# Optimization experiments

Hardware: AMD Instinct MI355X
Metric: run time of the kernel (lower is better)

Reference implementation:

```python
import jax, jax.numpy as jnp
import numpy as np
import math

DIM = 4096
N_HEADS = 32
HEAD_DIM = DIM // N_HEADS  # 128
SEQLEN = 2048


def setup_inputs() -> dict:
    key = jax.random.key(0)
    ks = jax.random.split(key, 8)
    x = jax.random.normal(ks[0], (1, SEQLEN, DIM), dtype=jnp.float32)
    # freqs_cis as real view: (seqlen, head_dim//2, 2) = (cos, sin) of rotary angles
    theta = 10000.0 ** (-jnp.arange(0, HEAD_DIM, 2, dtype=jnp.float32) / HEAD_DIM)
    angles = jnp.arange(SEQLEN, dtype=jnp.float32)[:, None] * theta[None, :]
    freqs = jnp.stack([jnp.cos(angles), jnp.sin(angles)], axis=-1)  # (S, 64, 2)
    # causal additive mask (use -1e9 instead of -inf for numeric safety)
    mask = jnp.triu(jnp.full((SEQLEN, SEQLEN), -1e9, dtype=jnp.float32), k=1)[None, None]
    scale = 1.0 / math.sqrt(DIM)
    wq = jax.random.normal(ks[1], (DIM, DIM), dtype=jnp.float32) * scale
    wk = jax.random.normal(ks[2], (DIM, DIM), dtype=jnp.float32) * scale
    wv = jax.random.normal(ks[3], (DIM, DIM), dtype=jnp.float32) * scale
    wo = jax.random.normal(ks[4], (DIM, DIM), dtype=jnp.float32) * scale
    return {"x": x, "start_pos": 0, "freqs": freqs, "mask": mask,
            "wq": wq, "wk": wk, "wv": wv, "wo": wo}


def _rotary(xq, xk, freqs, seqlen, n_heads, head_dim):
    # Faithful to source: note the repo's slice(0, 2) means xq_ == xq (no pair swap).
    ll = freqs[:, :, 0:1]  # (S, hd/2, 1) cos
    rr = freqs[:, :, 1:2]  # (S, hd/2, 1) sin
    fl = jnp.concatenate([ll, ll], axis=-1).reshape(seqlen, 1, head_dim)
    fr = jnp.concatenate([-rr, rr], axis=-1).reshape(seqlen, 1, head_dim)
    xq_ = xq.reshape(seqlen, n_heads, head_dim // 2, 2).reshape(seqlen, n_heads, head_dim)  # == xq
    xk_ = xk.reshape(seqlen, n_heads, head_dim // 2, 2).reshape(seqlen, n_heads, head_dim)  # == xk
    return xq * fl + xq_ * fr, xk * fl + xk_ * fr


def reference(x, start_pos, freqs, mask, wq, wk, wv, wo):
    bsz, seqlen, dim = x.shape  # bsz == 1 (source squeezes batch)
    xs = x[0]  # (S, D) -- HE encrypt/linear/decrypt roundtrip == plain linear
    xq = xs @ wq.T
    xk = xs @ wk.T
    xv = xs @ wv.T
    xq = xq.reshape(seqlen, N_HEADS, HEAD_DIM)
    xk = xk.reshape(seqlen, N_HEADS, HEAD_DIM)
    xv = xv.reshape(seqlen, N_HEADS, HEAD_DIM)
    xq, xk = _rotary(xq, xk, freqs, seqlen, N_HEADS, HEAD_DIM)
    # start_pos == 0 and zero-initialized cache => keys/values are just xk/xv
    q = jnp.transpose(xq, (1, 0, 2))  # (H, S, Dh)
    k = jnp.transpose(xk, (1, 0, 2))
    v = jnp.transpose(xv, (1, 0, 2))
    scores = jnp.einsum('hqd,hkd->hqk', q, k) / math.sqrt(HEAD_DIM)  # (H, S, S)
    scores = scores[None] + mask  # (1, H, S, S)
    probs = jax.nn.softmax(scores, axis=-1)
    out = jnp.einsum('bhqk,hkd->bhqd', probs, v)  # (1, H, S, Dh)
    out = jnp.transpose(out, (0, 2, 1, 3)).reshape(bsz, seqlen, dim)
    return out @ wo.T
```

## Files before the change

kernel.cpp:

```cpp
#include <hip/hip_runtime.h>

#define DIM 4096
#define SEQ 2048
#define NH 32
#define HD 128

typedef __bf16 bf16x8 __attribute__((ext_vector_type(8)));
typedef float f32x4 __attribute__((ext_vector_type(4)));

#define QSCALE 0.12751649736765598f

__device__ inline ushort f2bf(float f) {
    union { float f; unsigned u; } v; v.f = f;
    unsigned r = v.u + 0x7fffu + ((v.u >> 16) & 1u);
    return (ushort)(r >> 16);
}

__global__ void conv_all(const float* __restrict__ x,  const float* __restrict__ wq,
                         const float* __restrict__ wk, const float* __restrict__ wv,
                         const float* __restrict__ wo,
                         ushort* __restrict__ xb,  ushort* __restrict__ wqb,
                         ushort* __restrict__ wkb, ushort* __restrict__ wvb,
                         ushort* __restrict__ wob) {
    int i = blockIdx.x * 256 + threadIdx.x;
    const float* src; ushort* dst; int off;
    const int n4x = (SEQ * DIM) / 4;
    if (i < n4x) { src = x; dst = xb; off = i; }
    else {
        int j = i - n4x;
        int w = j >> 22;
        off = j & ((1 << 22) - 1);
        src = (w == 0) ? wq : (w == 1) ? wk : (w == 2) ? wv : wo;
        dst = (w == 0) ? wqb : (w == 1) ? wkb : (w == 2) ? wvb : wob;
    }
    float4 v = ((const float4*)src)[off];
    ushort4 o;
    o.x = f2bf(v.x); o.y = f2bf(v.y); o.z = f2bf(v.z); o.w = f2bf(v.w);
    ((ushort4*)dst)[off] = o;
}


#define AS1(p) (const __attribute__((address_space(1))) void*)(p)
#define AS3(p) (__attribute__((address_space(3))) void*)(p)
#define FENCE() asm volatile("" ::: "memory")
#define BARRIER() do { FENCE(); __builtin_amdgcn_s_barrier(); FENCE(); } while (0)

__device__ __forceinline__ void gemm256_body(
    const ushort* __restrict__ Ab,
    const ushort* __restrict__ Bb,
    ushort* __restrict__ sA0, ushort* __restrict__ sA1,
    ushort* __restrict__ sB0, ushort* __restrict__ sB1,
    f32x4 acc[8][4], const int K)
{
    const int tid  = threadIdx.x;
    const int wave = tid >> 6, lane = tid & 63;
    const int quad = lane >> 4, c = lane & 15;
    const int wm = wave >> 2, wn = wave & 3;

    const int aoff  = (lane >> 3) * K + (((lane & 7) ^ (lane >> 3)) * 8);
    const int sa_r0 = wave * 8;
    const int sb_r0 = (wave >> 1) * 64 + (wave & 1) * 16;

    const int rp0 = (quad ^ (c & 7)) * 8;
    const int rp1 = ((4 + quad) ^ (c & 7)) * 8;
    const int arow = (wm * 128 + c) * 64;
    const int brow = (wn * 64 + c) * 64;

#define STAGE_A(dst, h, k0) do { \
    const int _r0 = (h) * 64 + sa_r0; \
    __builtin_amdgcn_global_load_lds(AS1(Ab + (size_t)_r0 * K + (k0) + aoff), \
                                     AS3((dst) + _r0 * 64), 16, 0, 0); \
    const int _r1 = _r0 + 128; \
    __builtin_amdgcn_global_load_lds(AS1(Ab + (size_t)_r1 * K + (k0) + aoff), \
                                     AS3((dst) + _r1 * 64), 16, 0, 0); \
  } while (0)
#define STAGE_B(dst, h, k0) do { \
    const int _r0 = (h) * 32 + sb_r0; \
    __builtin_amdgcn_global_load_lds(AS1(Bb + (size_t)_r0 * K + (k0) + aoff), \
                                     AS3((dst) + _r0 * 64), 16, 0, 0); \
    const int _r1 = _r0 + 8; \
    __builtin_amdgcn_global_load_lds(AS1(Bb + (size_t)_r1 * K + (k0) + aoff), \
                                     AS3((dst) + _r1 * 64), 16, 0, 0); \
  } while (0)

    bf16x8 af[4][2], bfr[4][2];

#define READ_A(buf, mh) do { \
    _Pragma("unroll") \
    for (int _m = 0; _m < 4; ++_m) { \
        af[_m][0] = *(const bf16x8*)&(buf)[arow + (mh) * 4096 + _m * 1024 + rp0]; \
        af[_m][1] = *(const bf16x8*)&(buf)[arow + (mh) * 4096 + _m * 1024 + rp1]; \
    } } while (0)
#define READ_B2(buf, nh) do { \
    _Pragma("unroll") \
    for (int _n = 0; _n < 2; ++_n) { \
        bfr[(nh) * 2 + _n][0] = *(const bf16x8*)&(buf)[brow + (nh) * 2048 + _n * 1024 + rp0]; \
        bfr[(nh) * 2 + _n][1] = *(const bf16x8*)&(buf)[brow + (nh) * 2048 + _n * 1024 + rp1]; \
    } } while (0)
#define MMA_Q(mh, nq) do { \
    __builtin_amdgcn_s_setprio(1); \
    _Pragma("unroll") \
    for (int _kk = 0; _kk < 2; ++_kk) \
    _Pragma("unroll") \
    for (int _m = 0; _m < 4; ++_m) \
    _Pragma("unroll") \
    for (int _n = 0; _n < 2; ++_n) \
        acc[(mh) * 4 + _m][(nq) * 2 + _n] = __builtin_amdgcn_mfma_f32_16x16x32_bf16( \
            af[_m][_kk], bfr[(nq) * 2 + _n][_kk], acc[(mh) * 4 + _m][(nq) * 2 + _n], 0, 0, 0); \
    __builtin_amdgcn_s_setprio(0); \
  } while (0)

    const int NT = K >> 6;

    STAGE_A(sA0, 0, 0);  STAGE_A(sA0, 1, 0);
    STAGE_B(sB0, 0, 0);  STAGE_B(sB0, 1, 0);
    STAGE_A(sA1, 0, 64); STAGE_A(sA1, 1, 64);
    STAGE_B(sB1, 0, 64); STAGE_B(sB1, 1, 64);
    asm volatile("s_waitcnt vmcnt(8)" ::: "memory");
    BARRIER();

#pragma unroll 1
    for (int t = 0; t < NT; ++t) {
        ushort* cA = (t & 1) ? sA1 : sA0;
        ushort* cB = (t & 1) ? sB1 : sB0;
        const int kn2 = (t + 2) << 6;
        const bool ok2 = (t + 2 < NT);

        READ_A(cA, 0); READ_B2(cB, 0);
        BARRIER();
        MMA_Q(0, 0);
        BARRIER();

        READ_B2(cB, 1);
        if (ok2) { STAGE_A(cA, 0, kn2); STAGE_B(cB, 0, kn2); }
        BARRIER();
        MMA_Q(0, 1);
        BARRIER();

        READ_A(cA, 1);
        if (ok2) STAGE_B(cB, 1, kn2);
        BARRIER();
        MMA_Q(1, 0);
        BARRIER();

        if (ok2) STAGE_A(cA, 1, kn2);
        BARRIER();
        MMA_Q(1, 1);
        if (t < NT - 1) {
            if (ok2) asm volatile("s_waitcnt vmcnt(8)" ::: "memory");
            else     asm volatile("s_waitcnt vmcnt(0)" ::: "memory");
        }
        BARRIER();
    }
#undef STAGE_A
#undef STAGE_B
#undef READ_A
#undef READ_B2
#undef MMA_Q
}

__global__ __launch_bounds__(512, 2)
void gemm_qkv(const ushort* __restrict__ A,
              const ushort* __restrict__ Bq, const ushort* __restrict__ Bk,
              const ushort* __restrict__ Bv,
              ushort* __restrict__ qout, ushort* __restrict__ kout,
              ushort* __restrict__ vt, const float* __restrict__ freqs) {
    __shared__ __align__(16) ushort sA[2][256 * 64];
    __shared__ __align__(16) ushort sB[2][256 * 64];
    const int bi = blockIdx.x;
    const int x = bi & 7;
    const int l = bi >> 3;
    const int mblk = l & 7;
    const int nblk = x * 6 + (l >> 3);
    const int wsel = nblk >> 4;
    const int nloc = (nblk & 15) * 256;
    const int m0 = mblk * 256;
    const ushort* B = (wsel == 0) ? Bq : (wsel == 1) ? Bk : Bv;

    const f32x4 vzero = {0.f, 0.f, 0.f, 0.f};
    f32x4 acc[8][4];
#pragma unroll
    for (int i = 0; i < 8; i++)
#pragma unroll
        for (int j = 0; j < 4; j++) acc[i][j] = vzero;

    gemm256_body(A + (size_t)m0 * DIM, B + (size_t)nloc * DIM,
                 &sA[0][0], &sA[1][0], &sB[0][0], &sB[1][0], acc, DIM);

    const int tid = threadIdx.x;
    const int wave = tid >> 6, lane = tid & 63;
    const int quad = lane >> 4, c = lane & 15;
    const int wm = wave >> 2, wn = wave & 3;

    if (wsel < 2) {
        ushort* Cw = wsel ? kout : qout;
        const float qs = wsel ? 1.0f : QSCALE;
#pragma unroll
        for (int i = 0; i < 8; i++) {
#pragma unroll
            for (int j = 0; j < 4; j++) {
                int colg = nloc + wn * 64 + j * 16 + c;
                int dh = (colg & 127) >> 1;
#pragma unroll
                for (int r = 0; r < 4; r++) {
                    int row = m0 + wm * 128 + i * 16 + quad * 4 + r;
                    float2 f2 = ((const float2*)freqs)[row * 64 + dh];
                    float f = (f2.x + ((c & 1) ? f2.y : -f2.y)) * qs;
                    Cw[(size_t)row * DIM + colg] = f2bf(acc[i][j][r] * f);
                }
            }
        }
    } else {
#pragma unroll
        for (int i = 0; i < 8; i++) {
#pragma unroll
            for (int j = 0; j < 4; j++) {
                int cv = nloc + wn * 64 + j * 16 + c;
                int row0 = m0 + wm * 128 + i * 16 + quad * 4;
                ushort4 o;
                o.x = f2bf(acc[i][j][0]); o.y = f2bf(acc[i][j][1]);
                o.z = f2bf(acc[i][j][2]); o.w = f2bf(acc[i][j][3]);
                *(ushort4*)&vt[(size_t)cv * SEQ + row0] = o;
            }
        }
    }
}

__global__ __launch_bounds__(512, 2)
void gemm_f32out(const ushort* __restrict__ A, const ushort* __restrict__ B,
                 float* __restrict__ C, int M, int N, int K) {
    __shared__ __align__(16) ushort sA[2][256 * 64];
    __shared__ __align__(16) ushort sB[2][256 * 64];
    const int bi = blockIdx.x;
    const int x = bi & 7;
    const int l = bi >> 3;
    const int mblk = l & 7;
    const int nblk = x * 2 + (l >> 3);
    const int m0 = mblk * 256, n0 = nblk * 256;

    const f32x4 vzero = {0.f, 0.f, 0.f, 0.f};
    f32x4 acc[8][4];
#pragma unroll
    for (int i = 0; i < 8; i++)
#pragma unroll
        for (int j = 0; j < 4; j++) acc[i][j] = vzero;

    gemm256_body(A + (size_t)m0 * K, B + (size_t)n0 * K,
                 &sA[0][0], &sA[1][0], &sB[0][0], &sB[1][0], acc, K);

    const int tid = threadIdx.x;
    const int wave = tid >> 6, lane = tid & 63;
    const int quad = lane >> 4, c = lane & 15;
    const int wm = wave >> 2, wn = wave & 3;

#pragma unroll
    for (int i = 0; i < 8; i++)
#pragma unroll
        for (int j = 0; j < 4; j++)
#pragma unroll
            for (int r = 0; r < 4; r++) {
                int row = m0 + wm * 128 + i * 16 + quad * 4 + r;
                int col = n0 + wn * 64 + j * 16 + c;
                C[(size_t)row * N + col] = acc[i][j][r];
            }
}

__global__ __launch_bounds__(256)
void flash_kernel(const ushort* __restrict__ Q, const ushort* __restrict__ K,
                  const ushort* __restrict__ Vt, ushort* __restrict__ O) {
    const int bi = blockIdx.x;
    const int h = bi & (NH - 1);
    const int p = bi >> 5;
    __shared__ __align__(16) ushort sK[64 * 128];
    __shared__ __align__(16) ushort sVt[128 * 64];
    __shared__ __align__(16) ushort sP[4][16 * 72];
    const int tid = threadIdx.x, wave = tid >> 6, lane = tid & 63;
    const int quad = lane >> 4, c = lane & 15;

    for (int pass = 0; pass < 2; pass++) {
        const int qb = pass ? (SEQ / 64 - 1 - p) : p;
        const int q0 = qb * 64;

        bf16x8 qf[4];
        {
            const ushort* Qp = Q + (size_t)(q0 + wave * 16 + c) * DIM + h * HD;
#pragma unroll
            for (int ks = 0; ks < 4; ks++) qf[ks] = *(const bf16x8*)(Qp + ks * 32 + quad * 8);
        }
        const f32x4 vzero = {0.f, 0.f, 0.f, 0.f};
        f32x4 oa[8];
#pragma unroll
        for (int dt = 0; dt < 8; dt++) oa[dt] = vzero;
        float ms[4], ls[4];
#pragma unroll
        for (int r = 0; r < 4; r++) { ms[r] = -1e30f; ls[r] = 0.f; }

        for (int kt = 0; kt <= qb; kt++) {
            __syncthreads();
#pragma unroll
            for (int i = 0; i < 4; i++) {
                int lr = wave * 16 + i * 4 + (lane >> 4);
                int ch = lane & 15;
                int g = (ch & 8) | ((ch ^ lr) & 7);
                __builtin_amdgcn_global_load_lds(
                    (const __attribute__((address_space(1))) void*)(K + (size_t)(kt * 64 + lr) * DIM + h * HD + g * 8),
                    (__attribute__((address_space(3))) void*)(&sK[(wave * 16 + i * 4) * 128]), 16, 0, 0);
            }
#pragma unroll
            for (int i = 0; i < 4; i++) {
                int ld = wave * 32 + i * 8 + (lane >> 3);
                int ch = lane & 7;
                int g = (ch ^ ld) & 7;
                __builtin_amdgcn_global_load_lds(
                    (const __attribute__((address_space(1))) void*)(Vt + (size_t)(h * HD + ld) * SEQ + kt * 64 + g * 8),
                    (__attribute__((address_space(3))) void*)(&sVt[(wave * 32 + i * 8) * 64]), 16, 0, 0);
            }
            __syncthreads();

            f32x4 s[4];
#pragma unroll
            for (int nt = 0; nt < 4; nt++) s[nt] = vzero;
#pragma unroll
            for (int ks = 0; ks < 4; ks++)
#pragma unroll
                for (int nt = 0; nt < 4; nt++) {
                    int lr = nt * 16 + c;
                    int gc = ks * 4 + quad;
                    int pch = (gc & 8) | ((gc ^ lr) & 7);
                    bf16x8 kf = *(const bf16x8*)&sK[lr * 128 + pch * 8];
                    s[nt] = __builtin_amdgcn_mfma_f32_16x16x32_bf16(qf[ks], kf, s[nt], 0, 0, 0);
                }

            if (kt == qb) {
#pragma unroll
                for (int nt = 0; nt < 4; nt++)
#pragma unroll
                    for (int r = 0; r < 4; r++) {
                        int keyg = nt * 16 + c;
                        int qg   = wave * 16 + quad * 4 + r;
                        if (keyg > qg) s[nt][r] = -1e30f;
                    }
            }

            float mnew[4], alpha[4];
#pragma unroll
            for (int r = 0; r < 4; r++) {
                float v = fmaxf(fmaxf(s[0][r], s[1][r]), fmaxf(s[2][r], s[3][r]));
                v = fmaxf(v, __shfl_xor(v, 1));
                v = fmaxf(v, __shfl_xor(v, 2));
                v = fmaxf(v, __shfl_xor(v, 4));
                v = fmaxf(v, __shfl_xor(v, 8));
                mnew[r]  = fmaxf(ms[r], v);
                alpha[r] = exp2f(ms[r] - mnew[r]);
                ms[r]    = mnew[r];
            }
            float rs[4] = {0.f, 0.f, 0.f, 0.f};
#pragma unroll
            for (int nt = 0; nt < 4; nt++)
#pragma unroll
                for (int r = 0; r < 4; r++) {
                    float pv = exp2f(s[nt][r] - mnew[r]);
                    rs[r] += pv;
                    sP[wave][(quad * 4 + r) * 72 + nt * 16 + c] = f2bf(pv);
                }
#pragma unroll
            for (int r = 0; r < 4; r++) {
                float v = rs[r];
                v += __shfl_xor(v, 1);
                v += __shfl_xor(v, 2);
                v += __shfl_xor(v, 4);
                v += __shfl_xor(v, 8);
                ls[r] = ls[r] * alpha[r] + v;
            }
#pragma unroll
            for (int dt = 0; dt < 8; dt++)
#pragma unroll
                for (int r = 0; r < 4; r++) oa[dt][r] *= alpha[r];

            __asm__ volatile("s_waitcnt lgkmcnt(0)" ::: "memory");

#pragma unroll
            for (int k2 = 0; k2 < 2; k2++) {
                bf16x8 pf = *(const bf16x8*)&sP[wave][c * 72 + k2 * 32 + quad * 8];
#pragma unroll
                for (int dt = 0; dt < 8; dt++) {
                    int ld = dt * 16 + c;
                    int gc = k2 * 4 + quad;
                    int pch = (gc ^ ld) & 7;
                    bf16x8 vf = *(const bf16x8*)&sVt[ld * 64 + pch * 8];
                    oa[dt] = __builtin_amdgcn_mfma_f32_16x16x32_bf16(pf, vf, oa[dt], 0, 0, 0);
                }
            }
        }

#pragma unroll
        for (int r = 0; r < 4; r++) {
            float inv = 1.f / ls[r];
            int row = q0 + wave * 16 + quad * 4 + r;
#pragma unroll
            for (int dt = 0; dt < 8; dt++)
                O[(size_t)row * DIM + h * HD + dt * 16 + c] = f2bf(oa[dt][r] * inv);
        }
    }
}

extern "C" void kernel_launch(void* const* d_in, const int* in_sizes, int n_in,
                              void* d_out, int out_size, void* d_ws, size_t ws_size,
                              hipStream_t stream) {
    const float* x     = (const float*)d_in[0];
    const float* freqs = (const float*)d_in[2];
    const float* wq    = (const float*)d_in[4];
    const float* wk    = (const float*)d_in[5];
    const float* wv    = (const float*)d_in[6];
    const float* wo    = (const float*)d_in[7];
    float* out = (float*)d_out;

    ushort* xb    = (ushort*)d_ws;
    ushort* wqb   = xb    + (size_t)SEQ * DIM;
    ushort* wkb   = wqb   + (size_t)DIM * DIM;
    ushort* wvb   = wkb   + (size_t)DIM * DIM;
    ushort* wob   = wvb   + (size_t)DIM * DIM;
    ushort* qbuf  = wob   + (size_t)DIM * DIM;
    ushort* kbuf  = qbuf  + (size_t)SEQ * DIM;
    ushort* vtbuf = kbuf  + (size_t)SEQ * DIM;
    ushort* obuf  = vtbuf + (size_t)SEQ * DIM;

    const int n4tot = (SEQ * DIM + 4 * DIM * DIM) / 4;
    conv_all<<<n4tot / 256, 256, 0, stream>>>(x, wq, wk, wv, wo, xb, wqb, wkb, wvb, wob);

    gemm_qkv<<<dim3(384), 512, 0, stream>>>(xb, wqb, wkb, wvb, qbuf, kbuf, vtbuf, freqs);

    flash_kernel<<<dim3(NH * SEQ / 128), 256, 0, stream>>>(qbuf, kbuf, vtbuf, obuf);

    gemm_f32out<<<dim3(128), 512, 0, stream>>>(obuf, wob, out, SEQ, DIM, DIM);
}
```

Before: 759.3 us.

## Double-buffer K/V tiles in flash attention and raise MFMA wave priority

Gives the flash attention kernel two LDS buffers for K and V^T. The next key tile is prefetched with global_load_lds while the current tile is being computed, and partial vmcnt waits replace the per-iteration load-then-sync pattern. This is meant to hide global-memory latency behind the QK^T and PV MFMA work. It also wraps the MFMA loops in s_setprio so waves issue matrix work ahead of others. The cost is double the K/V LDS footprint, which may reduce the number of blocks resident per CU.

Measured after the change: 757.2 us. Within noise of the previous version (-0.3%).

```diff
diff --git a/kernel.cpp b/kernel.cpp
--- a/kernel.cpp
+++ b/kernel.cpp
@@ -271,12 +271,32 @@
     const int bi = blockIdx.x;
     const int h = bi & (NH - 1);
     const int p = bi >> 5;
-    __shared__ __align__(16) ushort sK[64 * 128];
-    __shared__ __align__(16) ushort sVt[128 * 64];
+    __shared__ __align__(16) ushort sK[2][64 * 128];
+    __shared__ __align__(16) ushort sVt[2][128 * 64];
     __shared__ __align__(16) ushort sP[4][16 * 72];
     const int tid = threadIdx.x, wave = tid >> 6, lane = tid & 63;
     const int quad = lane >> 4, c = lane & 15;
 
+#define STAGE_KV(db, kt) do { \
+    _Pragma("unroll") \
+    for (int _i = 0; _i < 4; _i++) { \
+        int _lr = wave * 16 + _i * 4 + (lane >> 4); \
+        int _ch = lane & 15; \
+        int _g = (_ch & 8) | ((_ch ^ _lr) & 7); \
+        __builtin_amdgcn_global_load_lds( \
+            AS1(K + (size_t)((kt) * 64 + _lr) * DIM + h * HD + _g * 8), \
+            AS3(&sK[db][(wave * 16 + _i * 4) * 128]), 16, 0, 0); \
+    } \
+    _Pragma("unroll") \
+    for (int _i = 0; _i < 4; _i++) { \
+        int _ld = wave * 32 + _i * 8 + (lane >> 3); \
+        int _ch = lane & 7; \
+        int _g = (_ch ^ _ld) & 7; \
+        __builtin_amdgcn_global_load_lds( \
+            AS1(Vt + (size_t)(h * HD + _ld) * SEQ + (kt) * 64 + _g * 8), \
+            AS3(&sVt[db][(wave * 32 + _i * 8) * 64]), 16, 0, 0); \
+    } } while (0)
+
     for (int pass = 0; pass < 2; pass++) {
         const int qb = pass ? (SEQ / 64 - 1 - p) : p;
         const int q0 = qb * 64;
@@ -295,31 +315,23 @@
 #pragma unroll
         for (int r = 0; r < 4; r++) { ms[r] = -1e30f; ls[r] = 0.f; }
 
+        STAGE_KV(0, 0);
+
+#pragma unroll 1
         for (int kt = 0; kt <= qb; kt++) {
-            __syncthreads();
-#pragma unroll
-            for (int i = 0; i < 4; i++) {
-                int lr = wave * 16 + i * 4 + (lane >> 4);
-                int ch = lane & 15;
-                int g = (ch & 8) | ((ch ^ lr) & 7);
-                __builtin_amdgcn_global_load_lds(
-                    (const __attribute__((address_space(1))) void*)(K + (size_t)(kt * 64 + lr) * DIM + h * HD + g * 8),
-                    (__attribute__((address_space(3))) void*)(&sK[(wave * 16 + i * 4) * 128]), 16, 0, 0);
-            }
-#pragma unroll
-            for (int i = 0; i < 4; i++) {
-                int ld = wave * 32 + i * 8 + (lane >> 3);
-                int ch = lane & 7;
-                int g = (ch ^ ld) & 7;
-                __builtin_amdgcn_global_load_lds(
-                    (const __attribute__((address_space(1))) void*)(Vt + (size_t)(h * HD + ld) * SEQ + kt * 64 + g * 8),
-                    (__attribute__((address_space(3))) void*)(&sVt[(wave * 32 + i * 8) * 64]), 16, 0, 0);
-            }
-            __syncthreads();
+            const int b = kt & 1;
+            if (kt < qb) {
+                STAGE_KV(b ^ 1, kt + 1);
+                asm volatile("s_waitcnt vmcnt(8)" ::: "memory");
+            } else {
+                asm volatile("s_waitcnt vmcnt(0)" ::: "memory");
+            }
+            BARRIER();
 
             f32x4 s[4];
 #pragma unroll
             for (int nt = 0; nt < 4; nt++) s[nt] = vzero;
+            __builtin_amdgcn_s_setprio(1);
 #pragma unroll
             for (int ks = 0; ks < 4; ks++)
 #pragma unroll
@@ -327,9 +339,10 @@
                     int lr = nt * 16 + c;
                     int gc = ks * 4 + quad;
                     int pch = (gc & 8) | ((gc ^ lr) & 7);
-                    bf16x8 kf = *(const bf16x8*)&sK[lr * 128 + pch * 8];
+                    bf16x8 kf = *(const bf16x8*)&sK[b][lr * 128 + pch * 8];
                     s[nt] = __builtin_amdgcn_mfma_f32_16x16x32_bf16(qf[ks], kf, s[nt], 0, 0, 0);
                 }
+            __builtin_amdgcn_s_setprio(0);
 
             if (kt == qb) {
 #pragma unroll
@@ -379,6 +392,7 @@
 
             __asm__ volatile("s_waitcnt lgkmcnt(0)" ::: "memory");
 
+            __builtin_amdgcn_s_setprio(1);
 #pragma unroll
             for (int k2 = 0; k2 < 2; k2++) {
                 bf16x8 pf = *(const bf16x8*)&sP[wave][c * 72 + k2 * 32 + quad * 8];
@@ -387,10 +401,13 @@
                     int ld = dt * 16 + c;
                     int gc = k2 * 4 + quad;
                     int pch = (gc ^ ld) & 7;
-                    bf16x8 vf = *(const bf16x8*)&sVt[ld * 64 + pch * 8];
+                    bf16x8 vf = *(const bf16x8*)&sVt[b][ld * 64 + pch * 8];
                     oa[dt] = __builtin_amdgcn_mfma_f32_16x16x32_bf16(pf, vf, oa[dt], 0, 0, 0);
                 }
             }
+            __builtin_amdgcn_s_setprio(0);
+
+            BARRIER();
         }
 
 #pragma unroll
@@ -402,6 +419,7 @@
                 O[(size_t)row * DIM + h * HD + dt * 16 + c] = f2bf(oa[dt][r] * inv);
         }
     }
+#undef STAGE_KV
 }
 
 extern "C" void kernel_launch(void* const* d_in, const int* in_sizes, int n_in,
```
